# Kernel tuning notes

Hardware: AMD Instinct MI355X
Metric: run time of the kernel (lower is better)

Reference implementation:

```python
import jax, jax.numpy as jnp
import numpy as np

FP8_MAX = 448.0  # float8_e4m3 max finite value


def setup_inputs() -> dict:
    key = jax.random.key(0)
    k1, k2, k3, k4, k5 = jax.random.split(key, 5)
    B, S, IN, OUT = 8, 2048, 2048, 2048
    x = jax.random.normal(k1, (B, S, IN), dtype=jnp.float32)
    weight = jax.random.normal(k2, (OUT, IN), dtype=jnp.float32) * 0.02
    bias = jax.random.normal(k3, (OUT,), dtype=jnp.float32)
    # per-tensor scales, kept positive and away from zero
    scale_in = jax.random.uniform(k4, (1,), dtype=jnp.float32) * 0.09 + 0.01
    scale_w = jax.random.uniform(k5, (1,), dtype=jnp.float32) * 0.09 + 0.01
    return {"x": x, "weight": weight, "bias": bias,
            "scale_in": scale_in, "scale_w": scale_w}


def _fp8_quantize(x, scale):
    # divide by scale, saturate to fp8 range, cast to fp8 e4m3
    q = jnp.clip(x / scale, -FP8_MAX, FP8_MAX)
    return q.astype(jnp.float8_e4m3fn)


def reference(x, weight, bias, scale_in, scale_w):
    # quantize input and weight to fp8 (per-tensor scales)
    xq = _fp8_quantize(x, scale_in)            # [B,S,IN] fp8
    wq = _fp8_quantize(weight, scale_w)        # [OUT,IN] fp8
    # scaled matmul: accumulate in fp32, dequant with scale_a*scale_b, emit fp16
    acc = jnp.einsum('bsk,nk->bsn', xq.astype(jnp.float32), wq.astype(jnp.float32))
    out = (acc * (scale_in[0] * scale_w[0])).astype(jnp.float16)
    out = out + bias.astype(jnp.float16)       # trailing bias add at fp16
    return out
```

## Files before the change

### kernel.cpp

```cpp
#include <hip/hip_runtime.h>
#include <hip/hip_fp16.h>
#include <stdint.h>

#define MDIM 16384
#define NDIM 2048
#define KDIM 2048

typedef __attribute__((ext_vector_type(4))) float f32x4;
typedef __attribute__((ext_vector_type(4))) int   i32x4;
typedef __attribute__((ext_vector_type(8))) int   i32x8;

#if defined(__has_builtin)
#if __has_builtin(__builtin_amdgcn_cvt_pk_fp8_f32)
#define HAVE_CVT_PK_FP8 1
#endif
#endif

__device__ __forceinline__ unsigned f32_to_e4m3(float x) {
    float q = fminf(448.f, fmaxf(-448.f, x));
    unsigned ub = __float_as_uint(q);
    unsigned sgn = (ub >> 24) & 0x80u;
    float aq = fabsf(q);
    int E = (int)((__float_as_uint(aq) >> 23) & 0xff) - 127;
    if (E < -6) E = -6;
    float rq = __uint_as_float((unsigned)(130 - E) << 23);
    int m = (int)rintf(aq * rq);
    if (m == 16) { m = 8; E += 1; }
    unsigned bits;
    if (m < 8) bits = sgn | (unsigned)m;
    else       bits = sgn | ((unsigned)(E + 7) << 3) | (unsigned)(m - 8);
    return bits;
}

__device__ __forceinline__ uint32_t pack4_e4m3(float a, float b, float c, float d) {
#ifdef HAVE_CVT_PK_FP8
    int r = __builtin_amdgcn_cvt_pk_fp8_f32(a, b, 0, false);
    r = __builtin_amdgcn_cvt_pk_fp8_f32(c, d, r, true);
    return (uint32_t)r;
#else
    return f32_to_e4m3(a) | (f32_to_e4m3(b) << 8) |
           (f32_to_e4m3(c) << 16) | (f32_to_e4m3(d) << 24);
#endif
}

__global__ void quant_both_kernel(const float* __restrict__ x,
                                  uint8_t* __restrict__ xq,
                                  const float* __restrict__ w,
                                  uint8_t* __restrict__ wq,
                                  const float* __restrict__ s_in,
                                  const float* __restrict__ s_w) {
    if (blockIdx.x < 2048) {
        float sc = s_in[0];
        unsigned n16 = (unsigned)((size_t)MDIM * KDIM / 16);
        unsigned i = blockIdx.x * 256 + threadIdx.x;
        for (; i < n16; i += 2048 * 256) {
            const float4* xp = (const float4*)(x + (size_t)i * 16);
            uint32_t wd[4];
#pragma unroll
            for (int j = 0; j < 4; ++j) {
                float4 v = xp[j];
                wd[j] = pack4_e4m3(v.x / sc, v.y / sc, v.z / sc, v.w / sc);
            }
            ((uint4*)xq)[i] = make_uint4(wd[0], wd[1], wd[2], wd[3]);
        }
    } else {
        float sc = s_w[0];
        unsigned n16 = (unsigned)((size_t)NDIM * KDIM / 16);
        unsigned i = (blockIdx.x - 2048) * 256 + threadIdx.x;
        for (; i < n16; i += 256 * 256) {
            const float4* xp = (const float4*)(w + (size_t)i * 16);
            uint32_t wd[4];
#pragma unroll
            for (int j = 0; j < 4; ++j) {
                float4 v = xp[j];
                wd[j] = pack4_e4m3(v.x / sc, v.y / sc, v.z / sc, v.w / sc);
            }
            unsigned r = i >> 7, kc = i & 127;
            unsigned idx = ((r >> 4) * 16 + (kc >> 3)) * 128 +
                           ((kc & 7) >> 1) * 32 + (r & 15) * 2 + (kc & 1);
            ((uint4*)wq)[idx] = make_uint4(wd[0], wd[1], wd[2], wd[3]);
        }
    }
}

#define BM 128
#define BN 256
#define BKB 128
#define NKT (KDIM / BKB)

__device__ __forceinline__ void gload_lds16(const uint8_t* g, uint8_t* l) {
    __builtin_amdgcn_global_load_lds(
        (const __attribute__((address_space(1))) void*)g,
        (__attribute__((address_space(3))) void*)l, 16, 0, 0);
}

__device__ __forceinline__ void barrier_raw() {
    asm volatile("" ::: "memory");
    __builtin_amdgcn_s_barrier();
    asm volatile("" ::: "memory");
}

__global__ __launch_bounds__(256, 2) void gemm_fp8_kernel(
    const uint8_t* __restrict__ Aq, const uint8_t* __restrict__ Bp,
    const float* __restrict__ bias, const float* __restrict__ s_in,
    const float* __restrict__ s_w, float* __restrict__ out) {

    extern __shared__ uint8_t lds[];

    int nwg = gridDim.x;
    int cpx = nwg >> 3;
    int bid = blockIdx.x;
    int swz = (bid & 7) * cpx + (bid >> 3);
    int tm = swz >> 3;
    int tn = swz & 7;
    int row0 = tm * BM;
    int col0 = tn * BN;

    int tid  = threadIdx.x;
    int lane = tid & 63;
    int wid  = tid >> 6;
    int wr = wid >> 1, wc = wid & 1;
    int r15 = lane & 15;
    int g   = lane >> 4;

    int perm0 = ((2 * g + r15) & 7) << 4;
    int perm1 = ((2 * g + 1 + r15) & 7) << 4;

    int ssrc[4], sdst[4];
#pragma unroll
    for (int i = 0; i < 4; ++i) {
        int p = i * 256 + tid;
        int lrow = p >> 3;
        int c = ((p & 7) - (lrow & 7)) & 7;
        ssrc[i] = lrow * KDIM + c * 16;
        sdst[i] = p * 16;
    }
    const uint8_t* Asrc = Aq + (size_t)row0 * KDIM;

#define STAGE_A(KT, BUF)                                                      \
    {                                                                         \
        _Pragma("unroll")                                                     \
        for (int j_ = 0; j_ < 4; ++j_)                                        \
            gload_lds16(Asrc + ssrc[j_] + (size_t)(KT) * BKB, (BUF) + sdst[j_]); \
    }

    const uint8_t* Bbase = Bp + (size_t)(tn * 16 + wc * 8) * 32768 + lane * 32;

#define LOAD_BF1(DST, N, KT)                                                  \
    {                                                                         \
        const uint8_t* p_ = Bbase + (size_t)(N) * 32768 + (size_t)(KT) * 2048; \
        i32x4 lo = *(const i32x4*)p_;                                         \
        i32x4 hi = *(const i32x4*)(p_ + 16);                                  \
        _Pragma("unroll")                                                     \
        for (int q_ = 0; q_ < 4; ++q_) { DST[q_] = lo[q_]; DST[4 + q_] = hi[q_]; } \
    }

#define LOAD_BF_ALL(KT)                                                       \
    LOAD_BF1(bf0, 0, KT); LOAD_BF1(bf1, 1, KT);                               \
    LOAD_BF1(bf2, 2, KT); LOAD_BF1(bf3, 3, KT);                               \
    LOAD_BF1(bf4, 4, KT); LOAD_BF1(bf5, 5, KT);                               \
    LOAD_BF1(bf6, 6, KT); LOAD_BF1(bf7, 7, KT);

    int aRow0 = wr * 64 + r15;

#define LOAD_AF1(DST, bo, M)                                                  \
    {                                                                         \
        const uint8_t* rp = lds + (bo) + (aRow0 + (M) * 16) * 128;            \
        i32x4 lo = *(const i32x4*)(rp + perm0);                               \
        i32x4 hi = *(const i32x4*)(rp + perm1);                               \
        _Pragma("unroll")                                                     \
        for (int q_ = 0; q_ < 4; ++q_) { DST[q_] = lo[q_]; DST[4 + q_] = hi[q_]; } \
    }

#define MFMA8(AF, M)                                                          \
    __builtin_amdgcn_s_setprio(1);                                            \
    acc[M][0] = __builtin_amdgcn_mfma_scale_f32_16x16x128_f8f6f4(             \
        AF, bf0, acc[M][0], 0, 0, 0, 127, 0, 127);                            \
    acc[M][1] = __builtin_amdgcn_mfma_scale_f32_16x16x128_f8f6f4(             \
        AF, bf1, acc[M][1], 0, 0, 0, 127, 0, 127);                            \
    acc[M][2] = __builtin_amdgcn_mfma_scale_f32_16x16x128_f8f6f4(             \
        AF, bf2, acc[M][2], 0, 0, 0, 127, 0, 127);                            \
    acc[M][3] = __builtin_amdgcn_mfma_scale_f32_16x16x128_f8f6f4(             \
        AF, bf3, acc[M][3], 0, 0, 0, 127, 0, 127);                            \
    acc[M][4] = __builtin_amdgcn_mfma_scale_f32_16x16x128_f8f6f4(             \
        AF, bf4, acc[M][4], 0, 0, 0, 127, 0, 127);                            \
    acc[M][5] = __builtin_amdgcn_mfma_scale_f32_16x16x128_f8f6f4(             \
        AF, bf5, acc[M][5], 0, 0, 0, 127, 0, 127);                            \
    acc[M][6] = __builtin_amdgcn_mfma_scale_f32_16x16x128_f8f6f4(             \
        AF, bf6, acc[M][6], 0, 0, 0, 127, 0, 127);                            \
    acc[M][7] = __builtin_amdgcn_mfma_scale_f32_16x16x128_f8f6f4(             \
        AF, bf7, acc[M][7], 0, 0, 0, 127, 0, 127);                            \
    __builtin_amdgcn_s_setprio(0);

    f32x4 acc[4][8];
#pragma unroll
    for (int m = 0; m < 4; ++m)
#pragma unroll
        for (int n = 0; n < 8; ++n)
            acc[m][n] = (f32x4){0.f, 0.f, 0.f, 0.f};

    i32x8 bf0, bf1, bf2, bf3, bf4, bf5, bf6, bf7;

    uint8_t* buf0 = &lds[0];
    uint8_t* buf1 = &lds[16384];

    STAGE_A(0, buf0);
    asm volatile("" ::: "memory");
    LOAD_BF_ALL(0);
    asm volatile("s_waitcnt vmcnt(16)" ::: "memory");
    barrier_raw();

#define TILE_BODY(T)                                                          \
    {                                                                         \
        const unsigned bo = ((unsigned)(T) & 1) << 14;                        \
        uint8_t* nxt_ = (((T) & 1) ? buf0 : buf1);                            \
        if ((T) + 1 < NKT) STAGE_A((T) + 1, nxt_);     \
        asm volatile("" ::: "memory");                                        \
        i32x8 afE, afO;                                                       \
        LOAD_AF1(afE, bo, 0);          \
        LOAD_AF1(afO, bo, 1); MFMA8(afE, 0);                                  \
        LOAD_AF1(afE, bo, 2); MFMA8(afO, 1);                                  \
        LOAD_AF1(afO, bo, 3); MFMA8(afE, 2);                                  \
                              MFMA8(afO, 3);                                  \
        if ((T) + 1 < NKT) {                                                  \
            LOAD_BF_ALL((T) + 1);                \
            asm volatile("s_waitcnt vmcnt(16)" ::: "memory");  \
        } else {                                                              \
            asm volatile("s_waitcnt vmcnt(0)" ::: "memory");                  \
        }                                                                     \
        barrier_raw();                                                        \
    }

    for (int t = 0; t < NKT; ++t)
        TILE_BODY(t);

    float s = s_in[0] * s_w[0];
    float* slab = (float*)lds;
    __half hb[8];
#pragma unroll
    for (int n = 0; n < 8; ++n)
        hb[n] = __float2half(bias[col0 + wc * 128 + n * 16 + r15]);

#pragma unroll
    for (int q = 0; q < 4; ++q) {
        if (wr == (q >> 1)) {
            const int mbase = 2 * (q & 1);
#pragma unroll
            for (int n = 0; n < 8; ++n) {
                int colb = wc * 128 + n * 16 + r15;
#pragma unroll
                for (int mm = 0; mm < 2; ++mm) {
                    int sr = mm * 16 + g * 4;
#pragma unroll
                    for (int r = 0; r < 4; ++r) {
                        __half h = __float2half(acc[mbase + mm][n][r] * s);
                        slab[(sr + r) * 256 + colb] = __half2float(__hadd(h, hb[n]));
                    }
                }
            }
        }
        barrier_raw();
#pragma unroll
        for (int it = 0; it < 8; ++it) {
            int srow = wid * 8 + it;
            f32x4 vv = *(const f32x4*)&slab[srow * 256 + lane * 4];
            int grow = row0 + q * 32 + srow;
            *(f32x4*)&out[(size_t)grow * NDIM + col0 + lane * 4] = vv;
        }
        barrier_raw();
    }
#undef STAGE_A
#undef LOAD_BF1
#undef LOAD_BF_ALL
#undef LOAD_AF1
#undef MFMA8
#undef TILE_BODY
}

extern "C" void kernel_launch(void* const* d_in, const int* in_sizes, int n_in,
                              void* d_out, int out_size, void* d_ws, size_t ws_size,
                              hipStream_t stream) {
    const float* x      = (const float*)d_in[0];
    const float* weight = (const float*)d_in[1];
    const float* bias   = (const float*)d_in[2];
    const float* s_in   = (const float*)d_in[3];
    const float* s_w    = (const float*)d_in[4];
    float* out          = (float*)d_out;

    uint8_t* xq = (uint8_t*)d_ws;
    uint8_t* wq = (uint8_t*)d_ws + (size_t)MDIM * KDIM;

    quant_both_kernel<<<2304, 256, 0, stream>>>(x, xq, weight, wq, s_in, s_w);

    dim3 grid((MDIM / BM) * (NDIM / BN));
    gemm_fp8_kernel<<<grid, 256, 32768, stream>>>(xq, wq, bias, s_in, s_w, out);
}
```

Baseline: 111.8 us.

## Stage two of eight B fragments through double-buffered LDS via async loads

Moves the last two B-fragment loads per wave (fragments 6 and 7) out of direct global-to-register loads and into a double-buffered LDS region filled with async global-to-LDS copies, shared by the waves that need the same columns. Fewer direct B loads stay in flight per thread, and the vmcnt waits are adjusted to match. This aims to cut duplicated global traffic and vector register pressure from B loads. In exchange it raises dynamic LDS from 32KB to 48KB per block, which may lower occupancy, and adds LDS reads before the MFMA chain.

```diff
diff --git a/kernel.cpp b/kernel.cpp
--- a/kernel.cpp
+++ b/kernel.cpp
@@ -144,6 +144,24 @@
             gload_lds16(Asrc + ssrc[j_] + (size_t)(KT) * BKB, (BUF) + sdst[j_]); \
     }
 
+    size_t bpsrc[2]; int bpdst[2];
+#pragma unroll
+    for (int j = 0; j < 2; ++j) {
+        int cj = j * 256 + tid;
+        int fj = cj >> 7;
+        int gfj = tn * 16 + (fj >> 1) * 8 + 6 + (fj & 1);
+        bpsrc[j] = (size_t)gfj * 32768 + (cj & 127) * 16;
+        bpdst[j] = cj * 16;
+    }
+
+#define STAGE_BP(KT, BO)                                                      \
+    {                                                                         \
+        _Pragma("unroll")                                                     \
+        for (int j_ = 0; j_ < 2; ++j_)                                        \
+            gload_lds16(Bp + bpsrc[j_] + (size_t)(KT) * 2048,                 \
+                        &lds[32768 + (BO)] + bpdst[j_]);                      \
+    }
+
     const uint8_t* Bbase = Bp + (size_t)(tn * 16 + wc * 8) * 32768 + lane * 32;
 
 #define LOAD_BF1(DST, N, KT)                                                  \
@@ -155,11 +173,22 @@
         for (int q_ = 0; q_ < 4; ++q_) { DST[q_] = lo[q_]; DST[4 + q_] = hi[q_]; } \
     }
 
-#define LOAD_BF_ALL(KT)                                                       \
-    LOAD_BF1(bf0, 0, KT); LOAD_BF1(bf1, 1, KT);                               \
-    LOAD_BF1(bf2, 2, KT); LOAD_BF1(bf3, 3, KT);                               \
-    LOAD_BF1(bf4, 4, KT); LOAD_BF1(bf5, 5, KT);                               \
-    LOAD_BF1(bf6, 6, KT); LOAD_BF1(bf7, 7, KT);
+#define LOAD_BF05(KT)                                                         \
+    LOAD_BF1(bf0, 0, KT); LOAD_BF1(bf1, 1, KT); LOAD_BF1(bf2, 2, KT);         \
+    LOAD_BF1(bf3, 3, KT); LOAD_BF1(bf4, 4, KT); LOAD_BF1(bf5, 5, KT);
+
+#define LOAD_BF67(BOB)                                                        \
+    {                                                                         \
+        const uint8_t* p6_ = lds + 32768 + (BOB) + (wc * 2 + 0) * 2048 + lane * 32; \
+        const uint8_t* p7_ = lds + 32768 + (BOB) + (wc * 2 + 1) * 2048 + lane * 32; \
+        i32x4 lo6 = *(const i32x4*)p6_; i32x4 hi6 = *(const i32x4*)(p6_ + 16); \
+        i32x4 lo7 = *(const i32x4*)p7_; i32x4 hi7 = *(const i32x4*)(p7_ + 16); \
+        _Pragma("unroll")                                                     \
+        for (int q_ = 0; q_ < 4; ++q_) {                                      \
+            bf6[q_] = lo6[q_]; bf6[4 + q_] = hi6[q_];                         \
+            bf7[q_] = lo7[q_]; bf7[4 + q_] = hi7[q_];                         \
+        }                                                                     \
+    }
 
     int aRow0 = wr * 64 + r15;
 
@@ -205,26 +234,31 @@
     uint8_t* buf1 = &lds[16384];
 
     STAGE_A(0, buf0);
+    STAGE_BP(0, 0u);
     asm volatile("" ::: "memory");
-    LOAD_BF_ALL(0);
-    asm volatile("s_waitcnt vmcnt(16)" ::: "memory");
+    LOAD_BF05(0);
+    asm volatile("s_waitcnt vmcnt(12)" ::: "memory");
     barrier_raw();
 
 #define TILE_BODY(T)                                                          \
     {                                                                         \
-        const unsigned bo = ((unsigned)(T) & 1) << 14;                        \
-        uint8_t* nxt_ = (((T) & 1) ? buf0 : buf1);                            \
-        if ((T) + 1 < NKT) STAGE_A((T) + 1, nxt_);     \
+        const unsigned bo  = ((unsigned)(T) & 1) << 14;                       \
+        const unsigned bob = ((unsigned)(T) & 1) << 13;                       \
+        if ((T) + 1 < NKT) {                                                  \
+            STAGE_A((T) + 1, (((T) & 1) ? buf0 : buf1));                      \
+            STAGE_BP((T) + 1, (((T) & 1) ? 0u : 8192u));                      \
+        }                                                                     \
         asm volatile("" ::: "memory");                                        \
+        LOAD_BF67(bob);                                                       \
         i32x8 afE, afO;                                                       \
-        LOAD_AF1(afE, bo, 0);          \
+        LOAD_AF1(afE, bo, 0);        \
         LOAD_AF1(afO, bo, 1); MFMA8(afE, 0);                                  \
         LOAD_AF1(afE, bo, 2); MFMA8(afO, 1);                                  \
         LOAD_AF1(afO, bo, 3); MFMA8(afE, 2);                                  \
                               MFMA8(afO, 3);                                  \
         if ((T) + 1 < NKT) {                                                  \
-            LOAD_BF_ALL((T) + 1);                \
-            asm volatile("s_waitcnt vmcnt(16)" ::: "memory");  \
+            LOAD_BF05((T) + 1);                  \
+            asm volatile("s_waitcnt vmcnt(12)" ::: "memory");     \
         } else {                                                              \
             asm volatile("s_waitcnt vmcnt(0)" ::: "memory");                  \
         }                                                                     \
@@ -270,8 +304,10 @@
         barrier_raw();
     }
 #undef STAGE_A
+#undef STAGE_BP
 #undef LOAD_BF1
-#undef LOAD_BF_ALL
+#undef LOAD_BF05
+#undef LOAD_BF67
 #undef LOAD_AF1
 #undef MFMA8
 #undef TILE_BODY
@@ -293,5 +329,5 @@
     quant_both_kernel<<<2304, 256, 0, stream>>>(x, xq, weight, wq, s_in, s_w);
 
     dim3 grid((MDIM / BM) * (NDIM / BN));
-    gemm_fp8_kernel<<<grid, 256, 32768, stream>>>(xq, wq, bias, s_in, s_w, out);
-}
+    gemm_fp8_kernel<<<grid, 256, 49152, stream>>>(xq, wq, bias, s_in, s_w, out);
+}
```

Measured after the change: 112.3 us. No clear change (+0.4%).

## Triple-buffer A tiles in LDS with prefetch distance of two

Applied to the files above, without the earlier changes.

Changes the A-operand LDS staging from double buffering to a three-slot ring, issuing global-to-LDS loads two k-tiles ahead. A tile's loads then have a full iteration of MFMA work to complete before the barrier, with waitcnt thresholds adjusted to match. The cost is 48KB of dynamic LDS per block instead of 32KB, which may lower occupancy, and it adds rotating offset bookkeeping.

```diff
diff --git a/kernel.cpp b/kernel.cpp
--- a/kernel.cpp
+++ b/kernel.cpp
@@ -137,11 +137,12 @@
     }
     const uint8_t* Asrc = Aq + (size_t)row0 * KDIM;
 
-#define STAGE_A(KT, BUF)                                                      \
+#define STAGE_A(KT, OFF)                                                      \
     {                                                                         \
         _Pragma("unroll")                                                     \
         for (int j_ = 0; j_ < 4; ++j_)                                        \
-            gload_lds16(Asrc + ssrc[j_] + (size_t)(KT) * BKB, (BUF) + sdst[j_]); \
+            gload_lds16(Asrc + ssrc[j_] + (size_t)(KT) * BKB,                 \
+                        lds + (OFF) + sdst[j_]);                              \
     }
 
     const uint8_t* Bbase = Bp + (size_t)(tn * 16 + wc * 8) * 32768 + lane * 32;
@@ -163,9 +164,9 @@
 
     int aRow0 = wr * 64 + r15;
 
-#define LOAD_AF1(DST, bo, M)                                                  \
+#define LOAD_AF1(DST, OFF, M)                                                 \
     {                                                                         \
-        const uint8_t* rp = lds + (bo) + (aRow0 + (M) * 16) * 128;            \
+        const uint8_t* rp = lds + (OFF) + (aRow0 + (M) * 16) * 128;           \
         i32x4 lo = *(const i32x4*)(rp + perm0);                               \
         i32x4 hi = *(const i32x4*)(rp + perm1);                               \
         _Pragma("unroll")                                                     \
@@ -201,38 +202,33 @@
 
     i32x8 bf0, bf1, bf2, bf3, bf4, bf5, bf6, bf7;
 
-    uint8_t* buf0 = &lds[0];
-    uint8_t* buf1 = &lds[16384];
-
-    STAGE_A(0, buf0);
+    STAGE_A(0, 0u);
     asm volatile("" ::: "memory");
     LOAD_BF_ALL(0);
-    asm volatile("s_waitcnt vmcnt(16)" ::: "memory");
+    asm volatile("" ::: "memory");
+    STAGE_A(1, 16384u);
+    asm volatile("s_waitcnt vmcnt(20)" ::: "memory");
     barrier_raw();
 
-#define TILE_BODY(T)                                                          \
-    {                                                                         \
-        const unsigned bo = ((unsigned)(T) & 1) << 14;                        \
-        uint8_t* nxt_ = (((T) & 1) ? buf0 : buf1);                            \
-        if ((T) + 1 < NKT) STAGE_A((T) + 1, nxt_);     \
-        asm volatile("" ::: "memory");                                        \
-        i32x8 afE, afO;                                                       \
-        LOAD_AF1(afE, bo, 0);          \
-        LOAD_AF1(afO, bo, 1); MFMA8(afE, 0);                                  \
-        LOAD_AF1(afE, bo, 2); MFMA8(afO, 1);                                  \
-        LOAD_AF1(afO, bo, 3); MFMA8(afE, 2);                                  \
-                              MFMA8(afO, 3);                                  \
-        if ((T) + 1 < NKT) {                                                  \
-            LOAD_BF_ALL((T) + 1);                \
-            asm volatile("s_waitcnt vmcnt(16)" ::: "memory");  \
-        } else {                                                              \
-            asm volatile("s_waitcnt vmcnt(0)" ::: "memory");                  \
-        }                                                                     \
-        barrier_raw();                                                        \
-    }
-
-    for (int t = 0; t < NKT; ++t)
-        TILE_BODY(t);
+    unsigned offCur = 0u, offNxt = 16384u, offNN = 32768u;
+
+    for (int t = 0; t < NKT; ++t) {
+        i32x8 afE, afO;
+        LOAD_AF1(afE, offCur, 0);
+        LOAD_AF1(afO, offCur, 1); MFMA8(afE, 0);
+        LOAD_AF1(afE, offCur, 2); MFMA8(afO, 1);
+        LOAD_AF1(afO, offCur, 3); MFMA8(afE, 2);
+                                  MFMA8(afO, 3);
+        asm volatile("" ::: "memory");
+        if (t + 1 < NKT) { LOAD_BF_ALL(t + 1); }
+        asm volatile("" ::: "memory");
+        if (t + 2 < NKT) { STAGE_A(t + 2, offNN); }
+        if (t + 2 < NKT)      asm volatile("s_waitcnt vmcnt(20)" ::: "memory");
+        else if (t + 1 < NKT) asm volatile("s_waitcnt vmcnt(16)" ::: "memory");
+        else                  asm volatile("s_waitcnt vmcnt(0)"  ::: "memory");
+        barrier_raw();
+        unsigned tmp_ = offCur; offCur = offNxt; offNxt = offNN; offNN = tmp_;
+    }
 
     float s = s_in[0] * s_w[0];
     float* slab = (float*)lds;
@@ -274,7 +270,6 @@
 #undef LOAD_BF_ALL
 #undef LOAD_AF1
 #undef MFMA8
-#undef TILE_BODY
 }
 
 extern "C" void kernel_launch(void* const* d_in, const int* in_sizes, int n_in,
@@ -293,5 +288,5 @@
     quant_both_kernel<<<2304, 256, 0, stream>>>(x, xq, weight, wq, s_in, s_w);
 
     dim3 grid((MDIM / BM) * (NDIM / BN));
-    gemm_fp8_kernel<<<grid, 256, 32768, stream>>>(xq, wq, bias, s_in, s_w, out);
-}
+    gemm_fp8_kernel<<<grid, 256, 49152, stream>>>(xq, wq, bias, s_in, s_w, out);
+}
```

New measurement: 125.4 us. 1.12x slower.
